# Performance work log

Hardware: AMD Instinct MI355X
Metric: run time of the kernel (lower is better)

Reference implementation:

```python
import jax, jax.numpy as jnp
import numpy as np

B, S, H, DH = 2, 4096, 8, 64
D = H * DH  # 512

def setup_inputs() -> dict:
    key = jax.random.key(0)
    ks = jax.random.split(key, 9)
    sc = 1.0 / np.sqrt(D)
    return {
        "hidden_states": jax.random.normal(ks[0], (B, S, D), jnp.float32),
        "Wq": jax.random.normal(ks[1], (D, D), jnp.float32) * sc,
        "bq": jax.random.normal(ks[2], (D,), jnp.float32) * 0.02,
        "Wk": jax.random.normal(ks[3], (D, D), jnp.float32) * sc,
        "bk": jax.random.normal(ks[4], (D,), jnp.float32) * 0.02,
        "Wv": jax.random.normal(ks[5], (D, D), jnp.float32) * sc,
        "bv": jax.random.normal(ks[6], (D,), jnp.float32) * 0.02,
        "Wo": jax.random.normal(ks[7], (D, D), jnp.float32) * sc,
        "bo": jax.random.normal(ks[8], (D,), jnp.float32) * 0.02,
    }

def _split_heads(t):
    # (B, S, H*DH) -> (B, H, S, DH)
    b = t.shape[0]
    return t.reshape(b, S, H, DH).transpose(0, 2, 1, 3)

def reference(hidden_states, Wq, bq, Wk, bk, Wv, bv, Wo, bo):
    q = _split_heads(hidden_states @ Wq + bq)
    k = _split_heads(hidden_states @ Wk + bk)
    v = _split_heads(hidden_states @ Wv + bv)
    scale = 1.0 / jnp.sqrt(jnp.asarray(DH, q.dtype))
    energy = jnp.einsum('bhqd,bhkd->bhqk', q, k) * scale
    weights = jax.nn.softmax(energy, axis=-1)  # full O(S^2) matrix, as in source
    attended = jnp.einsum('bhqv,bhvd->bhqd', weights, v)
    merged = attended.transpose(0, 2, 1, 3).reshape(hidden_states.shape[0], S, D)
    return merged @ Wo + bo
```

## Files before the change

### kernel.cpp

```cpp
#include <hip/hip_runtime.h>
#include <cstdint>

typedef __bf16 bf16;
typedef __bf16 bf16x4 __attribute__((ext_vector_type(4)));
typedef __bf16 bf16x8 __attribute__((ext_vector_type(8)));
typedef float floatx4 __attribute__((ext_vector_type(4)));

#define MFMA32(a, b, c) __builtin_amdgcn_mfma_f32_16x16x32_bf16((a), (b), (c), 0, 0, 0)

__device__ inline bf16x8 cvt8(const float* p) {
    float4 u = *(const float4*)p;
    float4 v = *(const float4*)(p + 4);
    bf16x8 r;
    r[0] = (bf16)u.x; r[1] = (bf16)u.y; r[2] = (bf16)u.z; r[3] = (bf16)u.w;
    r[4] = (bf16)v.x; r[5] = (bf16)v.y; r[6] = (bf16)v.z; r[7] = (bf16)v.w;
    return r;
}

__global__ __launch_bounds__(256) void k_transpose(
    const float* __restrict__ w0, const float* __restrict__ w1,
    const float* __restrict__ w2, const float* __restrict__ w3,
    bf16* __restrict__ o0, bf16* __restrict__ o1,
    bf16* __restrict__ o2, bf16* __restrict__ o3)
{
    __shared__ float t[32][33];
    const float* in;
    bf16* out;
    switch (blockIdx.z) {
        case 0: in = w0; out = o0; break;
        case 1: in = w1; out = o1; break;
        case 2: in = w2; out = o2; break;
        default: in = w3; out = o3; break;
    }
    const int tx = threadIdx.x & 31;
    const int ty = threadIdx.x >> 5;
    const int r0 = blockIdx.y * 32;
    const int c0 = blockIdx.x * 32;
    #pragma unroll
    for (int i = 0; i < 32; i += 8)
        t[ty + i][tx] = in[(size_t)(r0 + ty + i) * 512 + c0 + tx];
    __syncthreads();
    #pragma unroll
    for (int i = 0; i < 32; i += 8)
        out[(size_t)(c0 + ty + i) * 512 + r0 + tx] = (bf16)t[tx][ty + i];
}

__global__ __launch_bounds__(256) void k_cvtx(
    const float* __restrict__ X, bf16* __restrict__ Xb)
{
    const size_t idx = ((size_t)blockIdx.x * 256 + threadIdx.x) * 8;
    *(bf16x8*)(Xb + idx) = cvt8(X + idx);
}

__global__ __launch_bounds__(256) void k_qkv(
    const bf16* __restrict__ Xb, const bf16* __restrict__ Wcat,
    const float* __restrict__ bq, const float* __restrict__ bk, const float* __restrict__ bv,
    bf16* __restrict__ Qs, bf16* __restrict__ Ks, bf16* __restrict__ Vt)
{
    __shared__ __align__(16) unsigned char smem[36864];
    uint4* Al = (uint4*)smem;
    uint4* Bl = (uint4*)(smem + 16384);

    const int tid  = threadIdx.x;
    const int w    = tid >> 6;
    const int lane = tid & 63;
    const int col  = lane & 15;
    const int quad = lane >> 4;
    const int m0 = blockIdx.x * 128;
    const int n0 = blockIdx.y * 128;

    const bf16* gA0 = Xb   + (size_t)(m0 + (tid >> 2)) * 512 + (tid & 3) * 8;
    const bf16* gA1 = gA0 + 64 * 512;
    const bf16* gB0 = Wcat + (size_t)(n0 + (tid >> 2)) * 512 + (tid & 3) * 8;
    const bf16* gB1 = gB0 + 64 * 512;

    const floatx4 zf = {0.f, 0.f, 0.f, 0.f};
    floatx4 acc[4][4];
    #pragma unroll
    for (int a = 0; a < 4; ++a)
        #pragma unroll
        for (int b = 0; b < 4; ++b) acc[a][b] = zf;

    Al[tid]       = *(const uint4*)gA0;
    Al[tid + 256] = *(const uint4*)gA1;
    Bl[tid]       = *(const uint4*)gB0;
    Bl[tid + 256] = *(const uint4*)gB1;
    __syncthreads();

    const int mb = (w & 1) * 64;
    const int nb = (w >> 1) * 64;

    int buf = 0;
    for (int kk = 0; kk < 16; ++kk) {
        const int kn = ((kk + 1) & 15) * 32;
        const uint4 pa0 = *(const uint4*)(gA0 + kn);
        const uint4 pa1 = *(const uint4*)(gA1 + kn);
        const uint4 pb0 = *(const uint4*)(gB0 + kn);
        const uint4 pb1 = *(const uint4*)(gB1 + kn);

        const uint4* A4 = Al + buf * 512;
        const uint4* B4 = Bl + buf * 512;
        bf16x8 af[4], bfr[4];
        #pragma unroll
        for (int t = 0; t < 4; ++t) {
            union { uint4 u; bf16x8 v; } ca, cb;
            ca.u = A4[(mb + 16 * t + col) * 4 + quad];
            cb.u = B4[(nb + 16 * t + col) * 4 + quad];
            af[t] = ca.v;
            bfr[t] = cb.v;
        }
        #pragma unroll
        for (int tm = 0; tm < 4; ++tm)
            #pragma unroll
            for (int tn = 0; tn < 4; ++tn)
                acc[tm][tn] = MFMA32(af[tm], bfr[tn], acc[tm][tn]);

        const int nbuf = buf ^ 1;
        Al[nbuf * 512 + tid]       = pa0;
        Al[nbuf * 512 + tid + 256] = pa1;
        Bl[nbuf * 512 + tid]       = pb0;
        Bl[nbuf * 512 + tid + 256] = pb1;
        __syncthreads();
        buf = nbuf;
    }

    bf16* ep = (bf16*)smem + (size_t)w * 64 * 72;

    const int which = blockIdx.y >> 2;
    const int nbase = (blockIdx.y & 3) * 128 + nb;
    const int h  = nbase >> 6;
    const int mw = m0 + mb;
    const int b  = mw >> 12;
    const int s0 = mw & 4095;
    const float qsc = 0.125f * 1.44269504088896f;

    if (which == 2) {
        #pragma unroll
        for (int tn = 0; tn < 4; ++tn) {
            const int d = 16 * tn + col;
            const float bb = bv[nbase + d];
            #pragma unroll
            for (int tm = 0; tm < 4; ++tm) {
                union { bf16 e[4]; uint2 u; } pk;
                #pragma unroll
                for (int r = 0; r < 4; ++r) pk.e[r] = (bf16)(acc[tm][tn][r] + bb);
                *(uint2*)(ep + d * 72 + 16 * tm + 4 * quad) = pk.u;
            }
        }
    } else {
        const float* bias = (which == 0) ? bq : bk;
        const float sc = (which == 0) ? qsc : 1.0f;
        #pragma unroll
        for (int tn = 0; tn < 4; ++tn) {
            const int d = 16 * tn + col;
            const float bb = bias[nbase + d];
            #pragma unroll
            for (int tm = 0; tm < 4; ++tm)
                #pragma unroll
                for (int r = 0; r < 4; ++r)
                    ep[(16 * tm + 4 * quad + r) * 72 + d] = (bf16)((acc[tm][tn][r] + bb) * sc);
        }
    }

    asm volatile("" ::: "memory");

    const int rl = lane >> 3;
    const int ch = lane & 7;
    bf16* gbase;
    size_t rowstride;
    if (which == 2) {
        gbase = Vt + (((size_t)b * 8 + h) * 64) * 4096 + s0;
        rowstride = 4096;
    } else {
        bf16* P = (which == 0) ? Qs : Ks;
        gbase = P + (((size_t)b * 8 + h) * 4096 + s0) * 64;
        rowstride = 64;
    }
    #pragma unroll
    for (int it = 0; it < 8; ++it) {
        const int row = it * 8 + rl;
        const uint4 v = *(const uint4*)(ep + row * 72 + ch * 8);
        *(uint4*)(gbase + (size_t)row * rowstride + ch * 8) = v;
    }
}

__global__ __launch_bounds__(256) __attribute__((amdgpu_waves_per_eu(2, 2))) void k_attn(
    const bf16* __restrict__ Qs, const bf16* __restrict__ Ks, const bf16* __restrict__ Vt,
    bf16* __restrict__ att)
{
    __shared__ __align__(16) unsigned char smem[33280];
    uint4* Klds = (uint4*)smem;
    uint4* Vlds = (uint4*)(smem + 16384);
    float* Of   = (float*)smem;
    float* Ls   = (float*)(smem + 32768);

    const int tid  = threadIdx.x;
    const int w    = tid >> 6;
    const int hf   = w >> 1;
    const int wq   = w & 1;
    const int lane = tid & 63;
    const int col  = lane & 15;
    const int quad = lane >> 4;
    const int i    = blockIdx.x;
    const int bh   = ((i & 7) << 1) | ((i >> 3) & 1);
    const int q0   = (i >> 4) * 128 + wq * 64;

    const bf16* Qb = Qs + (size_t)bh * 262144;
    const bf16* Kb = Ks + (size_t)bh * 262144 + (size_t)hf * 2048 * 64;
    const bf16* Vb = Vt + (size_t)bh * 262144 + (size_t)hf * 2048;

    const int t7  = tid & 127;
    const int rK  = t7 >> 3;
    const int lcK = (t7 & 7) ^ (rK & 7);
    const bf16* gK = Kb + (size_t)rK * 64 + lcK * 8;
    const int pV  = t7 >> 3;
    const int ccV = (t7 & 7) ^ (pV & 7);
    const int dV  = 2 * pV + (ccV >> 2);
    const int cV  = ccV & 3;
    const bf16* gV = Vb + (size_t)dV * 4096 + cV * 8;

    uint4* Kl2 = Klds + hf * 512;
    uint4* Vl2 = Vlds + hf * 512;

    bf16x8 aq[4][2];
    #pragma unroll
    for (int s = 0; s < 4; ++s)
        #pragma unroll
        for (int c = 0; c < 2; ++c)
            aq[s][c] = *(const bf16x8*)(Qb + (size_t)(q0 + 16 * s + col) * 64 + 32 * c + quad * 8);

    const floatx4 zf = {0.f, 0.f, 0.f, 0.f};
    floatx4 o[4][4];
    float lsum[4] = {0.f, 0.f, 0.f, 0.f};
    #pragma unroll
    for (int s = 0; s < 4; ++s)
        #pragma unroll
        for (int dt = 0; dt < 4; ++dt) o[s][dt] = zf;

    const int c1 = col & 1, ch2 = col >> 1, qh = quad >> 1, ql = quad & 1;

    Kl2[t7]       = *(const uint4*)gK;
    Kl2[t7 + 128] = *(const uint4*)(gK + 1024);
    Vl2[t7]       = *(const uint4*)gV;
    Vl2[t7 + 128] = *(const uint4*)(gV + 131072);
    __syncthreads();

    int buf = 0;
    for (int kt = 0; kt < 2048; kt += 32) {
        const int kn = (kt + 32) & 2047;
        const uint4 kr0 = *(const uint4*)(gK + (size_t)kn * 64);
        const uint4 kr1 = *(const uint4*)(gK + (size_t)kn * 64 + 1024);
        const uint4 vr0 = *(const uint4*)(gV + kn);
        const uint4 vr1 = *(const uint4*)(gV + kn + 131072);

        const uint4* Kl = Kl2 + buf * 256;
        const uint2* Vl = (const uint2*)(Vl2 + buf * 256);

        bf16x8 kf[2][2];
        #pragma unroll
        for (int t = 0; t < 2; ++t)
            #pragma unroll
            for (int c = 0; c < 2; ++c) {
                union { uint4 u; bf16x8 v; } cv;
                cv.u = Kl[(16 * t + col) * 8 + ((quad + 4 * c) ^ (col & 7))];
                kf[t][c] = cv.v;
            }
        bf16x8 vfrag8[4];
        #pragma unroll
        for (int dt = 0; dt < 4; ++dt) {
            union { uint2 u[2]; bf16x8 v; } cv;
            #pragma unroll
            for (int t = 0; t < 2; ++t) {
                const int slot = (dt * 8 + ch2) * 8 + ((c1 * 4 + 2 * t + qh) ^ ch2);
                cv.u[t] = Vl[slot * 2 + ql];
            }
            vfrag8[dt] = cv.v;
        }

        #pragma unroll
        for (int s = 0; s < 4; ++s) {
            union { bf16 e[8]; bf16x8 v; } pw;
            #pragma unroll
            for (int t = 0; t < 2; ++t) {
                floatx4 sc = MFMA32(kf[t][1], aq[s][1], MFMA32(kf[t][0], aq[s][0], zf));
                const float p0 = __builtin_amdgcn_exp2f(sc[0]);
                const float p1 = __builtin_amdgcn_exp2f(sc[1]);
                const float p2 = __builtin_amdgcn_exp2f(sc[2]);
                const float p3 = __builtin_amdgcn_exp2f(sc[3]);
                lsum[s] += (p0 + p1) + (p2 + p3);
                pw.e[4 * t + 0] = (bf16)p0; pw.e[4 * t + 1] = (bf16)p1;
                pw.e[4 * t + 2] = (bf16)p2; pw.e[4 * t + 3] = (bf16)p3;
            }
            #pragma unroll
            for (int dt = 0; dt < 4; ++dt)
                o[s][dt] = MFMA32(vfrag8[dt], pw.v, o[s][dt]);
        }

        Kl2[(buf ^ 1) * 256 + t7]       = kr0;
        Kl2[(buf ^ 1) * 256 + t7 + 128] = kr1;
        Vl2[(buf ^ 1) * 256 + t7]       = vr0;
        Vl2[(buf ^ 1) * 256 + t7 + 128] = vr1;
        __syncthreads();
        buf ^= 1;
    }

    float lv[4];
    #pragma unroll
    for (int s = 0; s < 4; ++s) {
        float v = lsum[s];
        v += __shfl_xor(v, 16, 64);
        v += __shfl_xor(v, 32, 64);
        lv[s] = v;
    }

    float* op = Of + ((size_t)(wq * 64 + lane)) * 64;
    if (hf == 1) {
        #pragma unroll
        for (int s = 0; s < 4; ++s)
            #pragma unroll
            for (int dt = 0; dt < 4; ++dt) {
                const int f = s * 4 + dt;
                *(floatx4*)(op + ((f + lane) & 15) * 4) = o[s][dt];
            }
        if (quad == 0) {
            #pragma unroll
            for (int s = 0; s < 4; ++s)
                Ls[(wq * 4 + s) * 16 + col] = lv[s];
        }
    }
    __syncthreads();
    if (hf == 0) {
        float inv[4];
        #pragma unroll
        for (int s = 0; s < 4; ++s)
            inv[s] = 1.0f / (lv[s] + Ls[(wq * 4 + s) * 16 + col]);
        const int b  = bh >> 3;
        const int hh = bh & 7;
        #pragma unroll
        for (int s = 0; s < 4; ++s)
            #pragma unroll
            for (int dt = 0; dt < 4; ++dt) {
                const int f = s * 4 + dt;
                const floatx4 po = *(const floatx4*)(op + ((f + lane) & 15) * 4);
                union { bf16 e[4]; uint2 u; } pk;
                #pragma unroll
                for (int r = 0; r < 4; ++r)
                    pk.e[r] = (bf16)((o[s][dt][r] + po[r]) * inv[s]);
                const size_t row = (size_t)b * 4096 + q0 + 16 * s + col;
                *(uint2*)(att + row * 512 + hh * 64 + 16 * dt + 4 * quad) = pk.u;
            }
    }
}

__global__ __launch_bounds__(256) void k_oproj(
    const bf16* __restrict__ att, const bf16* __restrict__ Wto,
    const float* __restrict__ bo, float* __restrict__ out)
{
    __shared__ uint4 Al[2][512];
    __shared__ uint4 Bl[2][512];

    const int tid  = threadIdx.x;
    const int w    = tid >> 6;
    const int lane = tid & 63;
    const int col  = lane & 15;
    const int quad = lane >> 4;
    const int m0 = blockIdx.x * 128;
    const int n0 = blockIdx.y * 128;

    const bf16* gA0 = att + (size_t)(m0 + (tid >> 2)) * 512 + (tid & 3) * 8;
    const bf16* gA1 = gA0 + 64 * 512;
    const bf16* gB0 = Wto + (size_t)(n0 + (tid >> 2)) * 512 + (tid & 3) * 8;
    const bf16* gB1 = gB0 + 64 * 512;

    const floatx4 zf = {0.f, 0.f, 0.f, 0.f};
    floatx4 acc[4][4];
    #pragma unroll
    for (int a = 0; a < 4; ++a)
        #pragma unroll
        for (int b = 0; b < 4; ++b) acc[a][b] = zf;

    Al[0][tid]       = *(const uint4*)gA0;
    Al[0][tid + 256] = *(const uint4*)gA1;
    Bl[0][tid]       = *(const uint4*)gB0;
    Bl[0][tid + 256] = *(const uint4*)gB1;
    __syncthreads();

    const int mb = (w & 1) * 64;
    const int nb = (w >> 1) * 64;

    int buf = 0;
    for (int kk = 0; kk < 16; ++kk) {
        const int kn = ((kk + 1) & 15) * 32;
        const uint4 pa0 = *(const uint4*)(gA0 + kn);
        const uint4 pa1 = *(const uint4*)(gA1 + kn);
        const uint4 pb0 = *(const uint4*)(gB0 + kn);
        const uint4 pb1 = *(const uint4*)(gB1 + kn);

        const uint4* A4 = Al[buf];
        const uint4* B4 = Bl[buf];
        bf16x8 af[4], bfr[4];
        #pragma unroll
        for (int t = 0; t < 4; ++t) {
            union { uint4 u; bf16x8 v; } ca, cb;
            ca.u = A4[(mb + 16 * t + col) * 4 + quad];
            cb.u = B4[(nb + 16 * t + col) * 4 + quad];
            af[t] = ca.v;
            bfr[t] = cb.v;
        }
        #pragma unroll
        for (int tm = 0; tm < 4; ++tm)
            #pragma unroll
            for (int tn = 0; tn < 4; ++tn)
                acc[tm][tn] = MFMA32(af[tm], bfr[tn], acc[tm][tn]);

        Al[buf ^ 1][tid]       = pa0;
        Al[buf ^ 1][tid + 256] = pa1;
        Bl[buf ^ 1][tid]       = pb0;
        Bl[buf ^ 1][tid + 256] = pb1;
        __syncthreads();
        buf ^= 1;
    }

    #pragma unroll
    for (int tn = 0; tn < 4; ++tn) {
        const int n = n0 + nb + 16 * tn + col;
        const float bb = bo[n];
        #pragma unroll
        for (int tm = 0; tm < 4; ++tm)
            #pragma unroll
            for (int r = 0; r < 4; ++r) {
                const int m = m0 + mb + 16 * tm + quad * 4 + r;
                out[(size_t)m * 512 + n] = acc[tm][tn][r] + bb;
            }
    }
}

extern "C" void kernel_launch(void* const* d_in, const int* in_sizes, int n_in,
                              void* d_out, int out_size, void* d_ws, size_t ws_size,
                              hipStream_t stream)
{
    const float* X  = (const float*)d_in[0];
    const float* Wq = (const float*)d_in[1];
    const float* bq = (const float*)d_in[2];
    const float* Wk = (const float*)d_in[3];
    const float* bk = (const float*)d_in[4];
    const float* Wv = (const float*)d_in[5];
    const float* bv = (const float*)d_in[6];
    const float* Wo = (const float*)d_in[7];
    const float* bo = (const float*)d_in[8];

    bf16* Wtq = (bf16*)d_ws;
    bf16* Wtk = Wtq + 512 * 512;
    bf16* Wtv = Wtk + 512 * 512;
    bf16* Wto = Wtv + 512 * 512;
    bf16* Qs  = Wto + 512 * 512;
    bf16* Ks  = Qs + (size_t)16 * 4096 * 64;
    bf16* Vt  = Ks + (size_t)16 * 4096 * 64;
    bf16* att = Vt + (size_t)16 * 4096 * 64;

    bf16* Xb  = (bf16*)d_out;

    k_transpose<<<dim3(16, 16, 4), 256, 0, stream>>>(Wq, Wk, Wv, Wo, Wtq, Wtk, Wtv, Wto);
    k_cvtx<<<2048, 256, 0, stream>>>(X, Xb);
    k_qkv<<<dim3(64, 12), 256, 0, stream>>>(Xb, Wtq, bq, bk, bv, Qs, Ks, Vt);
    k_attn<<<512, 256, 0, stream>>>(Qs, Ks, Vt, att);
    k_oproj<<<dim3(64, 4), 256, 0, stream>>>(att, Wto, bo, (float*)d_out);
}
```

Measured before the change: 191.0 us.

## Split attention key range four ways per block with tree reduction

Measured after the change: 544.5 us. 185% more time.

```diff
diff --git a/kernel.cpp b/kernel.cpp
--- a/kernel.cpp
+++ b/kernel.cpp
@@ -184,19 +184,19 @@
     }
 }
 
-__global__ __launch_bounds__(256) __attribute__((amdgpu_waves_per_eu(2, 2))) void k_attn(
+__global__ __launch_bounds__(512) __attribute__((amdgpu_waves_per_eu(4, 4))) void k_attn(
     const bf16* __restrict__ Qs, const bf16* __restrict__ Ks, const bf16* __restrict__ Vt,
     bf16* __restrict__ att)
 {
-    __shared__ __align__(16) unsigned char smem[33280];
+    __shared__ __align__(16) unsigned char smem[66560];
     uint4* Klds = (uint4*)smem;
-    uint4* Vlds = (uint4*)(smem + 16384);
+    uint4* Vlds = (uint4*)(smem + 32768);
     float* Of   = (float*)smem;
-    float* Ls   = (float*)(smem + 32768);
+    float* Ls   = (float*)(smem + 65536);
 
     const int tid  = threadIdx.x;
     const int w    = tid >> 6;
-    const int hf   = w >> 1;
+    const int qt   = w >> 1;
     const int wq   = w & 1;
     const int lane = tid & 63;
     const int col  = lane & 15;
@@ -206,8 +206,8 @@
     const int q0   = (i >> 4) * 128 + wq * 64;
 
     const bf16* Qb = Qs + (size_t)bh * 262144;
-    const bf16* Kb = Ks + (size_t)bh * 262144 + (size_t)hf * 2048 * 64;
-    const bf16* Vb = Vt + (size_t)bh * 262144 + (size_t)hf * 2048;
+    const bf16* Kb = Ks + (size_t)bh * 262144 + (size_t)qt * 1024 * 64;
+    const bf16* Vb = Vt + (size_t)bh * 262144 + (size_t)qt * 1024;
 
     const int t7  = tid & 127;
     const int rK  = t7 >> 3;
@@ -219,8 +219,8 @@
     const int cV  = ccV & 3;
     const bf16* gV = Vb + (size_t)dV * 4096 + cV * 8;
 
-    uint4* Kl2 = Klds + hf * 512;
-    uint4* Vl2 = Vlds + hf * 512;
+    uint4* Kl2 = Klds + qt * 512;
+    uint4* Vl2 = Vlds + qt * 512;
 
     bf16x8 aq[4][2];
     #pragma unroll
@@ -246,8 +246,8 @@
     __syncthreads();
 
     int buf = 0;
-    for (int kt = 0; kt < 2048; kt += 32) {
-        const int kn = (kt + 32) & 2047;
+    for (int kt = 0; kt < 1024; kt += 32) {
+        const int kn = (kt + 32) & 1023;
         const uint4 kr0 = *(const uint4*)(gK + (size_t)kn * 64);
         const uint4 kr1 = *(const uint4*)(gK + (size_t)kn * 64 + 1024);
         const uint4 vr0 = *(const uint4*)(gV + kn);
@@ -313,35 +313,58 @@
         lv[s] = v;
     }
 
-    float* op = Of + ((size_t)(wq * 64 + lane)) * 64;
-    if (hf == 1) {
+    if (qt >= 2) {
+        const int r = (qt - 2) * 2 + wq;
+        float* op = Of + r * 4096 + lane * 64;
         #pragma unroll
         for (int s = 0; s < 4; ++s)
             #pragma unroll
-            for (int dt = 0; dt < 4; ++dt) {
-                const int f = s * 4 + dt;
-                *(floatx4*)(op + ((f + lane) & 15) * 4) = o[s][dt];
-            }
+            for (int dt = 0; dt < 4; ++dt)
+                *(floatx4*)(op + ((s * 4 + dt + lane) & 15) * 4) = o[s][dt];
         if (quad == 0) {
             #pragma unroll
-            for (int s = 0; s < 4; ++s)
-                Ls[(wq * 4 + s) * 16 + col] = lv[s];
-        }
-    }
-    __syncthreads();
-    if (hf == 0) {
+            for (int s = 0; s < 4; ++s) Ls[r * 64 + s * 16 + col] = lv[s];
+        }
+    }
+    __syncthreads();
+    if (qt <= 1) {
+        const int rr = qt * 2 + wq;
+        const float* op = Of + rr * 4096 + lane * 64;
+        #pragma unroll
+        for (int s = 0; s < 4; ++s) {
+            #pragma unroll
+            for (int dt = 0; dt < 4; ++dt)
+                o[s][dt] += *(const floatx4*)(op + ((s * 4 + dt + lane) & 15) * 4);
+            lv[s] += Ls[rr * 64 + s * 16 + col];
+        }
+    }
+    __syncthreads();
+    if (qt == 1) {
+        float* op = Of + wq * 4096 + lane * 64;
+        #pragma unroll
+        for (int s = 0; s < 4; ++s)
+            #pragma unroll
+            for (int dt = 0; dt < 4; ++dt)
+                *(floatx4*)(op + ((s * 4 + dt + lane) & 15) * 4) = o[s][dt];
+        if (quad == 0) {
+            #pragma unroll
+            for (int s = 0; s < 4; ++s) Ls[wq * 64 + s * 16 + col] = lv[s];
+        }
+    }
+    __syncthreads();
+    if (qt == 0) {
+        const float* op = Of + wq * 4096 + lane * 64;
         float inv[4];
         #pragma unroll
         for (int s = 0; s < 4; ++s)
-            inv[s] = 1.0f / (lv[s] + Ls[(wq * 4 + s) * 16 + col]);
+            inv[s] = 1.0f / (lv[s] + Ls[wq * 64 + s * 16 + col]);
         const int b  = bh >> 3;
         const int hh = bh & 7;
         #pragma unroll
         for (int s = 0; s < 4; ++s)
             #pragma unroll
             for (int dt = 0; dt < 4; ++dt) {
-                const int f = s * 4 + dt;
-                const floatx4 po = *(const floatx4*)(op + ((f + lane) & 15) * 4);
+                const floatx4 po = *(const floatx4*)(op + ((s * 4 + dt + lane) & 15) * 4);
                 union { bf16 e[4]; uint2 u; } pk;
                 #pragma unroll
                 for (int r = 0; r < 4; ++r)
@@ -463,6 +486,6 @@
     k_transpose<<<dim3(16, 16, 4), 256, 0, stream>>>(Wq, Wk, Wv, Wo, Wtq, Wtk, Wtv, Wto);
     k_cvtx<<<2048, 256, 0, stream>>>(X, Xb);
     k_qkv<<<dim3(64, 12), 256, 0, stream>>>(Xb, Wtq, bq, bk, bv, Qs, Ks, Vt);
-    k_attn<<<512, 256, 0, stream>>>(Qs, Ks, Vt, att);
+    k_attn<<<512, 512, 0, stream>>>(Qs, Ks, Vt, att);
     k_oproj<<<dim3(64, 4), 256, 0, stream>>>(att, Wto, bo, (float*)d_out);
 }
```
